# Performance work log

Hardware: AMD Instinct MI355X
Metric: run time of the kernel (lower is better)

The kernel has to match this reference:

```python
import jax, jax.numpy as jnp
import numpy as np

HIDDEN = 1024
HEADS = 16
HEAD_DIM = HIDDEN // HEADS  # 64
BATCH = 2
SEQ = 2048
MASK_IDENTITY = True


def setup_inputs() -> dict:
    key = jax.random.key(0)
    ks = jax.random.split(key, 9)
    s = 1.0 / np.sqrt(HIDDEN)
    return {
        "hidden_states": jax.random.normal(ks[0], (BATCH, SEQ, HIDDEN), jnp.float32),
        "Wq": jax.random.normal(ks[1], (HIDDEN, HIDDEN), jnp.float32) * s,
        "bq": jnp.zeros((HIDDEN,), jnp.float32),
        "Wk": jax.random.normal(ks[2], (HIDDEN, HIDDEN), jnp.float32) * s,
        "bk": jnp.zeros((HIDDEN,), jnp.float32),
        "Wv": jax.random.normal(ks[3], (HIDDEN, HIDDEN), jnp.float32) * s,
        "bv": jnp.zeros((HIDDEN,), jnp.float32),
        "Wd": jax.random.normal(ks[4], (HIDDEN, HIDDEN), jnp.float32) * s,
        "bd": jnp.zeros((HIDDEN,), jnp.float32),
    }


def _split_heads(x):
    # [B, S, H*Dh] -> [B, H, S, Dh]
    b, s, _ = x.shape
    return x.reshape(b, s, HEADS, HEAD_DIM).transpose(0, 2, 1, 3)


def reference(hidden_states, Wq, bq, Wk, bk, Wv, bv, Wd, bd):
    # torch Linear: y = x @ W.T + b
    q = _split_heads(hidden_states @ Wq.T + bq)  # [B,H,S,Dh]
    k = _split_heads(hidden_states @ Wk.T + bk)
    v = _split_heads(hidden_states @ Wv.T + bv)

    scores = jnp.einsum("bhqd,bhkd->bhqk", q, k) / np.sqrt(HEAD_DIM)
    if MASK_IDENTITY:
        mask_value = -jnp.finfo(scores.dtype).max
        eye = jnp.eye(scores.shape[-1], dtype=bool)  # [S,S], broadcast over B,H
        scores = jnp.where(eye, mask_value, scores)
    probs = jax.nn.softmax(scores, axis=-1)
    ctx = jnp.einsum("bhqk,bhkd->bhqd", probs, v)  # [B,H,S,Dh]
    b, h, s, d = ctx.shape
    ctx = ctx.transpose(0, 2, 1, 3).reshape(b, s, h * d)  # [B,S,H*Dh]
    return ctx @ Wd.T + bd
```

## Files before the change

kernel.cpp:

```cpp
#include <hip/hip_runtime.h>
#include <hip/hip_bf16.h>
#include <stdint.h>

#define HIDDEN 1024
#define SEQL   2048
#define NB     2
#define NH     16
#define DH     64
#define MTOT   (NB * SEQL)
#define QKVLD  3072
#define SCALE_Q 0.18033688011112042f

typedef __bf16 bf16x8 __attribute__((ext_vector_type(8)));
typedef __bf16 bf16x4 __attribute__((ext_vector_type(4)));
typedef float  f32x4  __attribute__((ext_vector_type(4)));
typedef float  f32x16 __attribute__((ext_vector_type(16)));

__device__ __forceinline__ void gload16(const void* g, void* l) {
    __builtin_amdgcn_global_load_lds(
        (const __attribute__((address_space(1))) void*)g,
        (__attribute__((address_space(3))) void*)l, 16, 0, 0);
}
__device__ __forceinline__ float exp2fast(float x) {
    float r;
    asm("v_exp_f32 %0, %1" : "=v"(r) : "v"(x));
    return r;
}
__device__ __forceinline__ unsigned cvtpk(float lo, float hi) {
    unsigned r;
    asm("v_cvt_pk_bf16_f32 %0, %1, %2" : "=v"(r) : "v"(lo), "v"(hi));
    return r;
}
__device__ __forceinline__ void pswap(unsigned& a, unsigned& b) {
    asm volatile("v_permlane32_swap_b32 %0, %1" : "+v"(a), "+v"(b));
}

__global__ void prep(const float* __restrict__ H,
                     const float* __restrict__ Wq, const float* __restrict__ Wk,
                     const float* __restrict__ Wv, const float* __restrict__ Wd,
                     const float* __restrict__ bq, const float* __restrict__ bk,
                     const float* __restrict__ bv,
                     __bf16* __restrict__ Hb, __bf16* __restrict__ Wall,
                     float* __restrict__ bqkv) {
    const int bid = blockIdx.x, tid = threadIdx.x;
    if (bid < 4096) {
        int i = bid * 256 + tid;
        float4 v = reinterpret_cast<const float4*>(H)[i];
        bf16x4 o = { (__bf16)v.x, (__bf16)v.y, (__bf16)v.z, (__bf16)v.w };
        reinterpret_cast<bf16x4*>(Hb)[i] = o;
    } else if (bid < 8192) {
        int wi = bid - 4096;
        int seg = wi >> 10;
        int i = (wi & 1023) * 256 + tid;
        const float* src = seg == 0 ? Wq : seg == 1 ? Wk : seg == 2 ? Wv : Wd;
        float sc = (seg == 0) ? SCALE_Q : 1.0f;
        float4 v = reinterpret_cast<const float4*>(src)[i];
        bf16x4 o = { (__bf16)(v.x * sc), (__bf16)(v.y * sc),
                     (__bf16)(v.z * sc), (__bf16)(v.w * sc) };
        reinterpret_cast<bf16x4*>(Wall)[(size_t)seg * 262144 + i] = o;
    } else {
        for (int i = tid; i < 3072; i += 256) {
            float v = (i < 1024) ? bq[i] * SCALE_Q
                    : (i < 2048) ? bk[i - 1024] : bv[i - 2048];
            bqkv[i] = v;
        }
    }
}

__global__ __launch_bounds__(256) void transpose_v(const __bf16* __restrict__ QKV,
                                                   __bf16* __restrict__ Vt) {
    __shared__ __bf16 t[64][66];
    const int st = blockIdx.x, bh = blockIdx.y;
    const int b = bh >> 4, h = bh & 15;
    const int tid = threadIdx.x;
    const int r = tid >> 3, c = tid & 7;
    const __bf16* src = QKV + (size_t)(b * SEQL + st * 64) * QKVLD + 2048 + h * 64;
    *(int4*)&t[r][c * 8]      = *(const int4*)(src + (size_t)r * QKVLD + c * 8);
    *(int4*)&t[r + 32][c * 8] = *(const int4*)(src + (size_t)(r + 32) * QKVLD + c * 8);
    __syncthreads();
    __bf16* dst = Vt + (size_t)bh * DH * SEQL + st * 64;
    const int d = tid >> 3;
    __bf16 tmp0[8], tmp1[8];
#pragma unroll
    for (int j = 0; j < 8; ++j) {
        tmp0[j] = t[c * 8 + j][d];
        tmp1[j] = t[c * 8 + j][d + 32];
    }
    *(int4*)(dst + (size_t)d * SEQL + c * 8)        = *(int4*)tmp0;
    *(int4*)(dst + (size_t)(d + 32) * SEQL + c * 8) = *(int4*)tmp1;
}

__global__ __launch_bounds__(256) void gemm_qkv(const __bf16* __restrict__ A,
                                                const __bf16* __restrict__ Bw,
                                                const float* __restrict__ bias,
                                                __bf16* __restrict__ C) {
    __shared__ __bf16 As[128 * 64];
    __shared__ __bf16 Bs[128 * 64];
    const int K = 1024, N = QKVLD;

    int bid = blockIdx.x;
    int swz = (bid & 7) * 96 + (bid >> 3);
    const int bm = (swz & 31) * 128;
    const int bn = (swz >> 5) * 128;

    const int tid = threadIdx.x;
    const int w = tid >> 6, l = tid & 63, g = l >> 4, lc = l & 15;
    const int wr = (w >> 1) * 64, wc = (w & 1) * 64;

    const int sr = l >> 3;
    const int scol = ((l & 7) ^ sr) * 8;
    const __bf16* Ap = A  + (size_t)(bm + w * 8 + sr) * K + scol;
    const __bf16* Bp = Bw + (size_t)(bn + w * 8 + sr) * K + scol;

    const int rswa = (lc & 7) * 8;

    f32x4 acc[4][4];
    const f32x4 z4 = {0.f, 0.f, 0.f, 0.f};
#pragma unroll
    for (int i = 0; i < 4; ++i)
#pragma unroll
        for (int j = 0; j < 4; ++j) acc[i][j] = z4;

    for (int kt = 0; kt < K; kt += 64) {
#pragma unroll
        for (int q = 0; q < 4; ++q) {
            gload16(Ap + kt + (size_t)(32 * q) * K, &As[(w * 8 + 32 * q) * 64]);
            gload16(Bp + kt + (size_t)(32 * q) * K, &Bs[(w * 8 + 32 * q) * 64]);
        }
        __syncthreads();

        bf16x8 af[4][2], bfr[4][2];
#pragma unroll
        for (int i = 0; i < 4; ++i) {
            const int ra = (wr + i * 16 + lc) * 64;
            const int rb = (wc + i * 16 + lc) * 64;
#pragma unroll
            for (int kk = 0; kk < 2; ++kk) {
                af[i][kk]  = *(const bf16x8*)&As[ra + ((kk * 32 + g * 8) ^ rswa)];
                bfr[i][kk] = *(const bf16x8*)&Bs[rb + ((kk * 32 + g * 8) ^ rswa)];
            }
        }
        __builtin_amdgcn_s_setprio(1);
#pragma unroll
        for (int kk = 0; kk < 2; ++kk)
#pragma unroll
            for (int i = 0; i < 4; ++i)
#pragma unroll
                for (int j = 0; j < 4; ++j)
                    acc[i][j] = __builtin_amdgcn_mfma_f32_16x16x32_bf16(af[i][kk], bfr[j][kk], acc[i][j], 0, 0, 0);
        __builtin_amdgcn_s_setprio(0);
        __syncthreads();
    }

#pragma unroll
    for (int i = 0; i < 4; ++i) {
        int r0 = bm + wr + i * 16 + g * 4;
#pragma unroll
        for (int j = 0; j < 4; ++j) {
            int c = bn + wc + j * 16 + lc;
            float bb = bias[c];
#pragma unroll
            for (int r = 0; r < 4; ++r)
                C[(size_t)(r0 + r) * N + c] = (__bf16)(acc[i][j][r] + bb);
        }
    }
}

__global__ __launch_bounds__(256) void gemm_out(const __bf16* __restrict__ A,
                                                const __bf16* __restrict__ Bw,
                                                const float* __restrict__ bias,
                                                float* __restrict__ Cout) {
    __shared__ __bf16 As[64 * 32];
    __shared__ __bf16 Bs[128 * 32];
    const int K = 1024, N = 1024;

    int bid = blockIdx.x;
    int swz = (bid & 7) * 64 + (bid >> 3);
    const int bm = (swz & 63) * 64;
    const int bn = (swz >> 6) * 128;

    const int tid = threadIdx.x;
    const int w = tid >> 6, l = tid & 63, g = l >> 4, lc = l & 15;
    const int wr = (w >> 1) * 32, wc = (w & 1) * 64;
    const int row = tid >> 2, ch = tid & 3;

    const __bf16* Ap = A  + (size_t)(bm + row) * K + ch * 8;
    const __bf16* Bp = Bw + (size_t)(bn + row) * K + ch * 8;
    __bf16* AsW  = &As[w * 512];
    __bf16* BsLo = &Bs[w * 512];
    __bf16* BsHi = &Bs[2048 + w * 512];

    f32x4 acc[2][4];
    const f32x4 z4 = {0.f, 0.f, 0.f, 0.f};
#pragma unroll
    for (int i = 0; i < 2; ++i)
#pragma unroll
        for (int j = 0; j < 4; ++j) acc[i][j] = z4;

    for (int kt = 0; kt < K; kt += 32) {
        gload16(Ap + kt,                   AsW);
        gload16(Bp + kt,                   BsLo);
        gload16(Bp + kt + (size_t)64 * K,  BsHi);
        __syncthreads();

        bf16x8 af[2], bfr[4];
#pragma unroll
        for (int i = 0; i < 2; ++i)
            af[i] = *(const bf16x8*)&As[(wr + i * 16 + lc) * 32 + g * 8];
#pragma unroll
        for (int j = 0; j < 4; ++j)
            bfr[j] = *(const bf16x8*)&Bs[(wc + j * 16 + lc) * 32 + g * 8];
        __builtin_amdgcn_s_setprio(1);
#pragma unroll
        for (int i = 0; i < 2; ++i)
#pragma unroll
            for (int j = 0; j < 4; ++j)
                acc[i][j] = __builtin_amdgcn_mfma_f32_16x16x32_bf16(af[i], bfr[j], acc[i][j], 0, 0, 0);
        __builtin_amdgcn_s_setprio(0);
        __syncthreads();
    }

#pragma unroll
    for (int i = 0; i < 2; ++i) {
        int r0 = bm + wr + i * 16 + g * 4;
#pragma unroll
        for (int j = 0; j < 4; ++j) {
            int c = bn + wc + j * 16 + lc;
            float bb = bias[c];
#pragma unroll
            for (int r = 0; r < 4; ++r)
                Cout[(size_t)(r0 + r) * N + c] = acc[i][j][r] + bb;
        }
    }
}

__global__ __launch_bounds__(256) void attn_kernel(const __bf16* __restrict__ QKV,
                                                   const __bf16* __restrict__ Vt,
                                                   __bf16* __restrict__ Ctx) {
    __shared__ __bf16 k_lds[2][128][64];
    __shared__ __bf16 v_lds[2][64][128];
    __shared__ float  bc[4][32];

    const int tid = threadIdx.x;
    const int w  = tid >> 6;
    const int l  = tid & 63;
    const int ql = l & 31;
    const int lh = l >> 5;

    int bid = blockIdx.x;
    int swz = (bid & 7) * 64 + (bid >> 3);
    const int qt = swz & 15, bh = swz >> 4;
    const int b = bh >> 4, hd = bh & 15;
    const int qw = qt * 128 + w * 32;

    const __bf16* Qg = QKV + (size_t)b * SEQL * QKVLD + hd * DH;
    const __bf16* Kg = Qg + 1024;
    const __bf16* Vg = Vt + (size_t)bh * DH * SEQL;

    bf16x8 qf[4];
    {
        const __bf16* qp = Qg + (size_t)(qw + ql) * QKVLD + lh * 8;
#pragma unroll
        for (int c = 0; c < 4; ++c) qf[c] = *(const bf16x8*)(qp + c * 16);
    }

    const int sr   = l >> 3;
    const int gcol = ((l & 7) ^ sr) * 8;
    const int vr  = l >> 4;
    const int vch = l & 15;

    auto stage = [&](int kb, int nb) {
#pragma unroll
        for (int q = 0; q < 4; ++q) {
            gload16(Kg + (size_t)(kb + w * 8 + 32 * q + sr) * QKVLD + gcol,
                    &k_lds[nb][w * 8 + 32 * q][0]);
        }
#pragma unroll
        for (int q = 0; q < 4; ++q) {
            int drow = w * 16 + 4 * q + vr;
            int vchunk = vch ^ (drow & 7);
            gload16(Vg + (size_t)drow * SEQL + kb + vchunk * 8,
                    &v_lds[nb][w * 16 + 4 * q][0]);
        }
    };

    stage(0, 0);
    __syncthreads();

    f32x16 o0, o1;
#pragma unroll
    for (int r = 0; r < 16; ++r) { o0[r] = 0.f; o1[r] = 0.f; }
    float l8[8];
#pragma unroll
    for (int r = 0; r < 8; ++r) l8[r] = 0.f;

    f32x16 zc;
#pragma unroll
    for (int r = 0; r < 16; ++r) zc[r] = 0.f;

    const int NT = SEQL / 128;
    const int rsw = (ql & 7) << 3;

    for (int kt = 0; kt < NT; ++kt) {
        const int buf = kt & 1;
        const int kb = kt * 128;

        if (kt + 1 < NT) stage(kb + 128, buf ^ 1);

#pragma unroll
        for (int sub = 0; sub < 2; ++sub) {
            const int kbs = kb + sub * 64;
            const int ro  = sub * 64;

            f32x16 sA, sB;
            __builtin_amdgcn_s_setprio(1);
            {
                bf16x8 k0 = *(const bf16x8*)&k_lds[buf][ro + ql]     [(lh * 8) ^ rsw];
                bf16x8 k1 = *(const bf16x8*)&k_lds[buf][ro + 32 + ql][(lh * 8) ^ rsw];
                sA = __builtin_amdgcn_mfma_f32_32x32x16_bf16(k0, qf[0], zc, 0, 0, 0);
                sB = __builtin_amdgcn_mfma_f32_32x32x16_bf16(k1, qf[0], zc, 0, 0, 0);
            }
#pragma unroll
            for (int c = 1; c < 4; ++c) {
                bf16x8 k0 = *(const bf16x8*)&k_lds[buf][ro + ql]     [(c * 16 + lh * 8) ^ rsw];
                bf16x8 k1 = *(const bf16x8*)&k_lds[buf][ro + 32 + ql][(c * 16 + lh * 8) ^ rsw];
                sA = __builtin_amdgcn_mfma_f32_32x32x16_bf16(k0, qf[c], sA, 0, 0, 0);
                sB = __builtin_amdgcn_mfma_f32_32x32x16_bf16(k1, qf[c], sB, 0, 0, 0);
            }
            __builtin_amdgcn_s_setprio(0);

            if (kbs < qw + 32 && qw < kbs + 64) {
                const int qg = qw + ql;
#pragma unroll
                for (int i = 0; i < 16; ++i) {
                    int kg = kbs + (i & 3) + ((i >> 2) & 3) * 8 + lh * 4;
                    if (kg == qg)      sA[i] = -1e30f;
                    if (kg + 32 == qg) sB[i] = -1e30f;
                }
            }

#pragma unroll
            for (int i = 0; i < 16; ++i) sA[i] = exp2fast(sA[i]);
#pragma unroll
            for (int i = 0; i < 16; ++i) sB[i] = exp2fast(sB[i]);
#pragma unroll
            for (int i = 0; i < 8; ++i)
                l8[i] += (sA[i] + sA[i + 8]) + (sB[i] + sB[i + 8]);

            bf16x8 pa[4];
            {
                unsigned w0 = cvtpk(sA[0],  sA[1]);
                unsigned w1 = cvtpk(sA[2],  sA[3]);
                unsigned w2 = cvtpk(sA[4],  sA[5]);
                unsigned w3 = cvtpk(sA[6],  sA[7]);
                unsigned w4 = cvtpk(sA[8],  sA[9]);
                unsigned w5 = cvtpk(sA[10], sA[11]);
                unsigned w6 = cvtpk(sA[12], sA[13]);
                unsigned w7 = cvtpk(sA[14], sA[15]);
                pswap(w0, w2); pswap(w1, w3);
                pswap(w4, w6); pswap(w5, w7);
                uint4 lo4 = {w0, w1, w2, w3};
                uint4 hi4 = {w4, w5, w6, w7};
                pa[0] = *(bf16x8*)&lo4;
                pa[1] = *(bf16x8*)&hi4;
            }
            {
                unsigned w0 = cvtpk(sB[0],  sB[1]);
                unsigned w1 = cvtpk(sB[2],  sB[3]);
                unsigned w2 = cvtpk(sB[4],  sB[5]);
                unsigned w3 = cvtpk(sB[6],  sB[7]);
                unsigned w4 = cvtpk(sB[8],  sB[9]);
                unsigned w5 = cvtpk(sB[10], sB[11]);
                unsigned w6 = cvtpk(sB[12], sB[13]);
                unsigned w7 = cvtpk(sB[14], sB[15]);
                pswap(w0, w2); pswap(w1, w3);
                pswap(w4, w6); pswap(w5, w7);
                uint4 lo4 = {w0, w1, w2, w3};
                uint4 hi4 = {w4, w5, w6, w7};
                pa[2] = *(bf16x8*)&lo4;
                pa[3] = *(bf16x8*)&hi4;
            }

            __builtin_amdgcn_s_setprio(1);
#pragma unroll
            for (int s = 0; s < 2; ++s)
#pragma unroll
                for (int sl = 0; sl < 2; ++sl) {
                    const int col = sub * 64 + s * 32 + sl * 16 + lh * 8;
                    bf16x8 v0 = *(const bf16x8*)&v_lds[buf][ql]     [col ^ rsw];
                    bf16x8 v1 = *(const bf16x8*)&v_lds[buf][32 + ql][col ^ rsw];
                    o0 = __builtin_amdgcn_mfma_f32_32x32x16_bf16(pa[s * 2 + sl], v0, o0, 0, 0, 0);
                    o1 = __builtin_amdgcn_mfma_f32_32x32x16_bf16(pa[s * 2 + sl], v1, o1, 0, 0, 0);
                }
            __builtin_amdgcn_s_setprio(0);
        }

        __syncthreads();
    }

    float l_r = ((l8[0] + l8[1]) + (l8[2] + l8[3]))
              + ((l8[4] + l8[5]) + (l8[6] + l8[7]));
    l_r += __shfl_xor(l_r, 32, 64);
    if (lh == 0) bc[w][ql] = 1.f / l_r;
    asm volatile("s_waitcnt lgkmcnt(0)" ::: "memory");
    __builtin_amdgcn_wave_barrier();
#pragma unroll
    for (int r = 0; r < 16; ++r) {
        int cr = (r & 3) + (r >> 2) * 8 + lh * 4;
        float iv = bc[w][cr];
        int qrow = qw + cr;
        __bf16* cp = Ctx + (size_t)(b * SEQL + qrow) * HIDDEN + hd * DH + ql;
        cp[0]  = (__bf16)(o0[r] * iv);
        cp[32] = (__bf16)(o1[r] * iv);
    }
}

extern "C" void kernel_launch(void* const* d_in, const int* in_sizes, int n_in,
                              void* d_out, int out_size, void* d_ws, size_t ws_size,
                              hipStream_t stream) {
    const float* H  = (const float*)d_in[0];
    const float* Wq = (const float*)d_in[1];
    const float* bq = (const float*)d_in[2];
    const float* Wk = (const float*)d_in[3];
    const float* bk = (const float*)d_in[4];
    const float* Wv = (const float*)d_in[5];
    const float* bv = (const float*)d_in[6];
    const float* Wd = (const float*)d_in[7];
    const float* bd = (const float*)d_in[8];
    float* out = (float*)d_out;

    char* ws = (char*)d_ws;
    const size_t MB = 1024 * 1024;
    __bf16* Hb    = (__bf16*)(ws + 0 * MB);
    __bf16* Ctx   = (__bf16*)(ws + 0 * MB);
    __bf16* Wqkvb = (__bf16*)(ws + 8 * MB);
    __bf16* Wdb   = (__bf16*)(ws + 14 * MB);
    float*  bqkv  = (float*) (ws + 16 * MB);
    __bf16* QKV   = (__bf16*)(ws + 17 * MB);
    __bf16* Vtb   = (__bf16*)(ws + 41 * MB);
    if (ws_size < 49 * MB) return;

    prep<<<8193, 256, 0, stream>>>(H, Wq, Wk, Wv, Wd, bq, bk, bv, Hb, Wqkvb, bqkv);

    gemm_qkv<<<768, 256, 0, stream>>>(Hb, Wqkvb, bqkv, QKV);

    transpose_v<<<dim3(32, 32), 256, 0, stream>>>(QKV, Vtb);

    attn_kernel<<<512, 256, 0, stream>>>(QKV, Vtb, Ctx);

    gemm_out<<<512, 256, 0, stream>>>(Ctx, Wdb, bd, out);
}
```

Before: 128.6 us.

## Double per-wave query rows in attention; shrink QKV GEMM K-tile to 32

The attention kernel now has each wave handle 64 query rows (two 32-row groups) instead of 32, so every K/V fragment read from shared memory feeds twice as many MFMAs. The grid is halved to 256 blocks of 256 queries each. Separately, the QKV GEMM now stages 32-wide K tiles without the XOR swizzle, halving shared memory but doubling the number of barrier iterations. Risks include higher register pressure in attention, only 256 blocks to fill the device, and possible LDS bank conflicts in the GEMM.

```diff
diff --git a/kernel.cpp b/kernel.cpp
--- a/kernel.cpp
+++ b/kernel.cpp
@@ -94,8 +94,8 @@
                                                 const __bf16* __restrict__ Bw,
                                                 const float* __restrict__ bias,
                                                 __bf16* __restrict__ C) {
-    __shared__ __bf16 As[128 * 64];
-    __shared__ __bf16 Bs[128 * 64];
+    __shared__ __bf16 As[128 * 32];
+    __shared__ __bf16 Bs[128 * 32];
     const int K = 1024, N = QKVLD;
 
     int bid = blockIdx.x;
@@ -106,13 +106,14 @@
     const int tid = threadIdx.x;
     const int w = tid >> 6, l = tid & 63, g = l >> 4, lc = l & 15;
     const int wr = (w >> 1) * 64, wc = (w & 1) * 64;
-
-    const int sr = l >> 3;
-    const int scol = ((l & 7) ^ sr) * 8;
-    const __bf16* Ap = A  + (size_t)(bm + w * 8 + sr) * K + scol;
-    const __bf16* Bp = Bw + (size_t)(bn + w * 8 + sr) * K + scol;
-
-    const int rswa = (lc & 7) * 8;
+    const int row = tid >> 2, ch = tid & 3;
+
+    const __bf16* Ap = A  + (size_t)(bm + row) * K + ch * 8;
+    const __bf16* Bp = Bw + (size_t)(bn + row) * K + ch * 8;
+    __bf16* AsLo = &As[w * 512];
+    __bf16* AsHi = &As[2048 + w * 512];
+    __bf16* BsLo = &Bs[w * 512];
+    __bf16* BsHi = &Bs[2048 + w * 512];
 
     f32x4 acc[4][4];
     const f32x4 z4 = {0.f, 0.f, 0.f, 0.f};
@@ -121,33 +122,26 @@
 #pragma unroll
         for (int j = 0; j < 4; ++j) acc[i][j] = z4;
 
-    for (int kt = 0; kt < K; kt += 64) {
-#pragma unroll
-        for (int q = 0; q < 4; ++q) {
-            gload16(Ap + kt + (size_t)(32 * q) * K, &As[(w * 8 + 32 * q) * 64]);
-            gload16(Bp + kt + (size_t)(32 * q) * K, &Bs[(w * 8 + 32 * q) * 64]);
-        }
+    for (int kt = 0; kt < K; kt += 32) {
+        gload16(Ap + kt,                   AsLo);
+        gload16(Ap + kt + (size_t)64 * K,  AsHi);
+        gload16(Bp + kt,                   BsLo);
+        gload16(Bp + kt + (size_t)64 * K,  BsHi);
         __syncthreads();
 
-        bf16x8 af[4][2], bfr[4][2];
-#pragma unroll
-        for (int i = 0; i < 4; ++i) {
-            const int ra = (wr + i * 16 + lc) * 64;
-            const int rb = (wc + i * 16 + lc) * 64;
-#pragma unroll
-            for (int kk = 0; kk < 2; ++kk) {
-                af[i][kk]  = *(const bf16x8*)&As[ra + ((kk * 32 + g * 8) ^ rswa)];
-                bfr[i][kk] = *(const bf16x8*)&Bs[rb + ((kk * 32 + g * 8) ^ rswa)];
-            }
-        }
+        bf16x8 af[4], bfr[4];
+#pragma unroll
+        for (int i = 0; i < 4; ++i)
+            af[i] = *(const bf16x8*)&As[(wr + i * 16 + lc) * 32 + g * 8];
+#pragma unroll
+        for (int j = 0; j < 4; ++j)
+            bfr[j] = *(const bf16x8*)&Bs[(wc + j * 16 + lc) * 32 + g * 8];
         __builtin_amdgcn_s_setprio(1);
 #pragma unroll
-        for (int kk = 0; kk < 2; ++kk)
-#pragma unroll
-            for (int i = 0; i < 4; ++i)
-#pragma unroll
-                for (int j = 0; j < 4; ++j)
-                    acc[i][j] = __builtin_amdgcn_mfma_f32_16x16x32_bf16(af[i][kk], bfr[j][kk], acc[i][j], 0, 0, 0);
+        for (int i = 0; i < 4; ++i)
+#pragma unroll
+            for (int j = 0; j < 4; ++j)
+                acc[i][j] = __builtin_amdgcn_mfma_f32_16x16x32_bf16(af[i], bfr[j], acc[i][j], 0, 0, 0);
         __builtin_amdgcn_s_setprio(0);
         __syncthreads();
     }
@@ -239,7 +233,7 @@
                                                    __bf16* __restrict__ Ctx) {
     __shared__ __bf16 k_lds[2][128][64];
     __shared__ __bf16 v_lds[2][64][128];
-    __shared__ float  bc[4][32];
+    __shared__ float  bc[4][64];
 
     const int tid = threadIdx.x;
     const int w  = tid >> 6;
@@ -248,27 +242,30 @@
     const int lh = l >> 5;
 
     int bid = blockIdx.x;
-    int swz = (bid & 7) * 64 + (bid >> 3);
-    const int qt = swz & 15, bh = swz >> 4;
+    int swz = (bid & 7) * 32 + (bid >> 3);
+    const int qt = swz & 7, bh = swz >> 3;
     const int b = bh >> 4, hd = bh & 15;
-    const int qw = qt * 128 + w * 32;
+    const int qw = qt * 256 + w * 64;
 
     const __bf16* Qg = QKV + (size_t)b * SEQL * QKVLD + hd * DH;
     const __bf16* Kg = Qg + 1024;
     const __bf16* Vg = Vt + (size_t)bh * DH * SEQL;
 
-    bf16x8 qf[4];
+    bf16x8 qfa[4], qfb[4];
     {
-        const __bf16* qp = Qg + (size_t)(qw + ql) * QKVLD + lh * 8;
-#pragma unroll
-        for (int c = 0; c < 4; ++c) qf[c] = *(const bf16x8*)(qp + c * 16);
+        const __bf16* qp0 = Qg + (size_t)(qw + ql) * QKVLD + lh * 8;
+        const __bf16* qp1 = Qg + (size_t)(qw + 32 + ql) * QKVLD + lh * 8;
+#pragma unroll
+        for (int c = 0; c < 4; ++c) {
+            qfa[c] = *(const bf16x8*)(qp0 + c * 16);
+            qfb[c] = *(const bf16x8*)(qp1 + c * 16);
+        }
     }
 
     const int sr   = l >> 3;
     const int gcol = ((l & 7) ^ sr) * 8;
     const int vr  = l >> 4;
     const int vch = l & 15;
-
     auto stage = [&](int kb, int nb) {
 #pragma unroll
         for (int q = 0; q < 4; ++q) {
@@ -287,12 +284,12 @@
     stage(0, 0);
     __syncthreads();
 
-    f32x16 o0, o1;
-#pragma unroll
-    for (int r = 0; r < 16; ++r) { o0[r] = 0.f; o1[r] = 0.f; }
-    float l8[8];
-#pragma unroll
-    for (int r = 0; r < 8; ++r) l8[r] = 0.f;
+    f32x16 oa0, oa1, ob0, ob1;
+#pragma unroll
+    for (int r = 0; r < 16; ++r) { oa0[r] = 0.f; oa1[r] = 0.f; ob0[r] = 0.f; ob1[r] = 0.f; }
+    float l8a[8], l8b[8];
+#pragma unroll
+    for (int r = 0; r < 8; ++r) { l8a[r] = 0.f; l8b[r] = 0.f; }
 
     f32x16 zc;
 #pragma unroll
@@ -312,20 +309,25 @@
             const int kbs = kb + sub * 64;
             const int ro  = sub * 64;
 
-            f32x16 sA, sB;
+            bf16x8 kf0[4], kf1[4];
+#pragma unroll
+            for (int c = 0; c < 4; ++c) {
+                kf0[c] = *(const bf16x8*)&k_lds[buf][ro + ql]     [(c * 16 + lh * 8) ^ rsw];
+                kf1[c] = *(const bf16x8*)&k_lds[buf][ro + 32 + ql][(c * 16 + lh * 8) ^ rsw];
+            }
+
+            f32x16 sA0, sB0, sA1, sB1;
             __builtin_amdgcn_s_setprio(1);
-            {
-                bf16x8 k0 = *(const bf16x8*)&k_lds[buf][ro + ql]     [(lh * 8) ^ rsw];
-                bf16x8 k1 = *(const bf16x8*)&k_lds[buf][ro + 32 + ql][(lh * 8) ^ rsw];
-                sA = __builtin_amdgcn_mfma_f32_32x32x16_bf16(k0, qf[0], zc, 0, 0, 0);
-                sB = __builtin_amdgcn_mfma_f32_32x32x16_bf16(k1, qf[0], zc, 0, 0, 0);
-            }
+            sA0 = __builtin_amdgcn_mfma_f32_32x32x16_bf16(kf0[0], qfa[0], zc, 0, 0, 0);
+            sB0 = __builtin_amdgcn_mfma_f32_32x32x16_bf16(kf1[0], qfa[0], zc, 0, 0, 0);
+            sA1 = __builtin_amdgcn_mfma_f32_32x32x16_bf16(kf0[0], qfb[0], zc, 0, 0, 0);
+            sB1 = __builtin_amdgcn_mfma_f32_32x32x16_bf16(kf1[0], qfb[0], zc, 0, 0, 0);
 #pragma unroll
             for (int c = 1; c < 4; ++c) {
-                bf16x8 k0 = *(const bf16x8*)&k_lds[buf][ro + ql]     [(c * 16 + lh * 8) ^ rsw];
-                bf16x8 k1 = *(const bf16x8*)&k_lds[buf][ro + 32 + ql][(c * 16 + lh * 8) ^ rsw];
-                sA = __builtin_amdgcn_mfma_f32_32x32x16_bf16(k0, qf[c], sA, 0, 0, 0);
-                sB = __builtin_amdgcn_mfma_f32_32x32x16_bf16(k1, qf[c], sB, 0, 0, 0);
+                sA0 = __builtin_amdgcn_mfma_f32_32x32x16_bf16(kf0[c], qfa[c], sA0, 0, 0, 0);
+                sB0 = __builtin_amdgcn_mfma_f32_32x32x16_bf16(kf1[c], qfa[c], sB0, 0, 0, 0);
+                sA1 = __builtin_amdgcn_mfma_f32_32x32x16_bf16(kf0[c], qfb[c], sA1, 0, 0, 0);
+                sB1 = __builtin_amdgcn_mfma_f32_32x32x16_bf16(kf1[c], qfb[c], sB1, 0, 0, 0);
             }
             __builtin_amdgcn_s_setprio(0);
 
@@ -334,51 +336,102 @@
 #pragma unroll
                 for (int i = 0; i < 16; ++i) {
                     int kg = kbs + (i & 3) + ((i >> 2) & 3) * 8 + lh * 4;
-                    if (kg == qg)      sA[i] = -1e30f;
-                    if (kg + 32 == qg) sB[i] = -1e30f;
+                    if (kg == qg)      sA0[i] = -1e30f;
+                    if (kg + 32 == qg) sB0[i] = -1e30f;
                 }
             }
-
-#pragma unroll
-            for (int i = 0; i < 16; ++i) sA[i] = exp2fast(sA[i]);
-#pragma unroll
-            for (int i = 0; i < 16; ++i) sB[i] = exp2fast(sB[i]);
+            if (kbs < qw + 64 && qw + 32 < kbs + 64) {
+                const int qg = qw + 32 + ql;
+#pragma unroll
+                for (int i = 0; i < 16; ++i) {
+                    int kg = kbs + (i & 3) + ((i >> 2) & 3) * 8 + lh * 4;
+                    if (kg == qg)      sA1[i] = -1e30f;
+                    if (kg + 32 == qg) sB1[i] = -1e30f;
+                }
+            }
+
+#pragma unroll
+            for (int i = 0; i < 16; ++i) sA0[i] = exp2fast(sA0[i]);
+#pragma unroll
+            for (int i = 0; i < 16; ++i) sB0[i] = exp2fast(sB0[i]);
 #pragma unroll
             for (int i = 0; i < 8; ++i)
-                l8[i] += (sA[i] + sA[i + 8]) + (sB[i] + sB[i + 8]);
-
-            bf16x8 pa[4];
+                l8a[i] += (sA0[i] + sA0[i + 8]) + (sB0[i] + sB0[i + 8]);
+
+            bf16x8 pa0[4];
             {
-                unsigned w0 = cvtpk(sA[0],  sA[1]);
-                unsigned w1 = cvtpk(sA[2],  sA[3]);
-                unsigned w2 = cvtpk(sA[4],  sA[5]);
-                unsigned w3 = cvtpk(sA[6],  sA[7]);
-                unsigned w4 = cvtpk(sA[8],  sA[9]);
-                unsigned w5 = cvtpk(sA[10], sA[11]);
-                unsigned w6 = cvtpk(sA[12], sA[13]);
-                unsigned w7 = cvtpk(sA[14], sA[15]);
+                unsigned w0 = cvtpk(sA0[0],  sA0[1]);
+                unsigned w1 = cvtpk(sA0[2],  sA0[3]);
+                unsigned w2 = cvtpk(sA0[4],  sA0[5]);
+                unsigned w3 = cvtpk(sA0[6],  sA0[7]);
+                unsigned w4 = cvtpk(sA0[8],  sA0[9]);
+                unsigned w5 = cvtpk(sA0[10], sA0[11]);
+                unsigned w6 = cvtpk(sA0[12], sA0[13]);
+                unsigned w7 = cvtpk(sA0[14], sA0[15]);
                 pswap(w0, w2); pswap(w1, w3);
                 pswap(w4, w6); pswap(w5, w7);
                 uint4 lo4 = {w0, w1, w2, w3};
                 uint4 hi4 = {w4, w5, w6, w7};
-                pa[0] = *(bf16x8*)&lo4;
-                pa[1] = *(bf16x8*)&hi4;
+                pa0[0] = *(bf16x8*)&lo4;
+                pa0[1] = *(bf16x8*)&hi4;
             }
             {
-                unsigned w0 = cvtpk(sB[0],  sB[1]);
-                unsigned w1 = cvtpk(sB[2],  sB[3]);
-                unsigned w2 = cvtpk(sB[4],  sB[5]);
-                unsigned w3 = cvtpk(sB[6],  sB[7]);
-                unsigned w4 = cvtpk(sB[8],  sB[9]);
-                unsigned w5 = cvtpk(sB[10], sB[11]);
-                unsigned w6 = cvtpk(sB[12], sB[13]);
-                unsigned w7 = cvtpk(sB[14], sB[15]);
+                unsigned w0 = cvtpk(sB0[0],  sB0[1]);
+                unsigned w1 = cvtpk(sB0[2],  sB0[3]);
+                unsigned w2 = cvtpk(sB0[4],  sB0[5]);
+                unsigned w3 = cvtpk(sB0[6],  sB0[7]);
+                unsigned w4 = cvtpk(sB0[8],  sB0[9]);
+                unsigned w5 = cvtpk(sB0[10], sB0[11]);
+                unsigned w6 = cvtpk(sB0[12], sB0[13]);
+                unsigned w7 = cvtpk(sB0[14], sB0[15]);
                 pswap(w0, w2); pswap(w1, w3);
                 pswap(w4, w6); pswap(w5, w7);
                 uint4 lo4 = {w0, w1, w2, w3};
                 uint4 hi4 = {w4, w5, w6, w7};
-                pa[2] = *(bf16x8*)&lo4;
-                pa[3] = *(bf16x8*)&hi4;
+                pa0[2] = *(bf16x8*)&lo4;
+                pa0[3] = *(bf16x8*)&hi4;
+            }
+
+#pragma unroll
+            for (int i = 0; i < 16; ++i) sA1[i] = exp2fast(sA1[i]);
+#pragma unroll
+            for (int i = 0; i < 16; ++i) sB1[i] = exp2fast(sB1[i]);
+#pragma unroll
+            for (int i = 0; i < 8; ++i)
+                l8b[i] += (sA1[i] + sA1[i + 8]) + (sB1[i] + sB1[i + 8]);
+
+            bf16x8 pa1[4];
+            {
+                unsigned w0 = cvtpk(sA1[0],  sA1[1]);
+                unsigned w1 = cvtpk(sA1[2],  sA1[3]);
+                unsigned w2 = cvtpk(sA1[4],  sA1[5]);
+                unsigned w3 = cvtpk(sA1[6],  sA1[7]);
+                unsigned w4 = cvtpk(sA1[8],  sA1[9]);
+                unsigned w5 = cvtpk(sA1[10], sA1[11]);
+                unsigned w6 = cvtpk(sA1[12], sA1[13]);
+                unsigned w7 = cvtpk(sA1[14], sA1[15]);
+                pswap(w0, w2); pswap(w1, w3);
+                pswap(w4, w6); pswap(w5, w7);
+                uint4 lo4 = {w0, w1, w2, w3};
+                uint4 hi4 = {w4, w5, w6, w7};
+                pa1[0] = *(bf16x8*)&lo4;
+                pa1[1] = *(bf16x8*)&hi4;
+            }
+            {
+                unsigned w0 = cvtpk(sB1[0],  sB1[1]);
+                unsigned w1 = cvtpk(sB1[2],  sB1[3]);
+                unsigned w2 = cvtpk(sB1[4],  sB1[5]);
+                unsigned w3 = cvtpk(sB1[6],  sB1[7]);
+                unsigned w4 = cvtpk(sB1[8],  sB1[9]);
+                unsigned w5 = cvtpk(sB1[10], sB1[11]);
+                unsigned w6 = cvtpk(sB1[12], sB1[13]);
+                unsigned w7 = cvtpk(sB1[14], sB1[15]);
+                pswap(w0, w2); pswap(w1, w3);
+                pswap(w4, w6); pswap(w5, w7);
+                uint4 lo4 = {w0, w1, w2, w3};
+                uint4 hi4 = {w4, w5, w6, w7};
+                pa1[2] = *(bf16x8*)&lo4;
+                pa1[3] = *(bf16x8*)&hi4;
             }
 
             __builtin_amdgcn_s_setprio(1);
@@ -389,8 +442,10 @@
                     const int col = sub * 64 + s * 32 + sl * 16 + lh * 8;
                     bf16x8 v0 = *(const bf16x8*)&v_lds[buf][ql]     [col ^ rsw];
                     bf16x8 v1 = *(const bf16x8*)&v_lds[buf][32 + ql][col ^ rsw];
-                    o0 = __builtin_amdgcn_mfma_f32_32x32x16_bf16(pa[s * 2 + sl], v0, o0, 0, 0, 0);
-                    o1 = __builtin_amdgcn_mfma_f32_32x32x16_bf16(pa[s * 2 + sl], v1, o1, 0, 0, 0);
+                    oa0 = __builtin_amdgcn_mfma_f32_32x32x16_bf16(pa0[s * 2 + sl], v0, oa0, 0, 0, 0);
+                    oa1 = __builtin_amdgcn_mfma_f32_32x32x16_bf16(pa0[s * 2 + sl], v1, oa1, 0, 0, 0);
+                    ob0 = __builtin_amdgcn_mfma_f32_32x32x16_bf16(pa1[s * 2 + sl], v0, ob0, 0, 0, 0);
+                    ob1 = __builtin_amdgcn_mfma_f32_32x32x16_bf16(pa1[s * 2 + sl], v1, ob1, 0, 0, 0);
                 }
             __builtin_amdgcn_s_setprio(0);
         }
@@ -398,20 +453,29 @@
         __syncthreads();
     }
 
-    float l_r = ((l8[0] + l8[1]) + (l8[2] + l8[3]))
-              + ((l8[4] + l8[5]) + (l8[6] + l8[7]));
-    l_r += __shfl_xor(l_r, 32, 64);
-    if (lh == 0) bc[w][ql] = 1.f / l_r;
+    float la = ((l8a[0] + l8a[1]) + (l8a[2] + l8a[3]))
+             + ((l8a[4] + l8a[5]) + (l8a[6] + l8a[7]));
+    float lb = ((l8b[0] + l8b[1]) + (l8b[2] + l8b[3]))
+             + ((l8b[4] + l8b[5]) + (l8b[6] + l8b[7]));
+    la += __shfl_xor(la, 32, 64);
+    lb += __shfl_xor(lb, 32, 64);
+    if (lh == 0) {
+        bc[w][ql]      = 1.f / la;
+        bc[w][32 + ql] = 1.f / lb;
+    }
     asm volatile("s_waitcnt lgkmcnt(0)" ::: "memory");
     __builtin_amdgcn_wave_barrier();
 #pragma unroll
     for (int r = 0; r < 16; ++r) {
         int cr = (r & 3) + (r >> 2) * 8 + lh * 4;
-        float iv = bc[w][cr];
-        int qrow = qw + cr;
-        __bf16* cp = Ctx + (size_t)(b * SEQL + qrow) * HIDDEN + hd * DH + ql;
-        cp[0]  = (__bf16)(o0[r] * iv);
-        cp[32] = (__bf16)(o1[r] * iv);
+        float iva = bc[w][cr];
+        float ivb = bc[w][32 + cr];
+        __bf16* cpa = Ctx + (size_t)(b * SEQL + qw + cr) * HIDDEN + hd * DH + ql;
+        __bf16* cpb = Ctx + (size_t)(b * SEQL + qw + 32 + cr) * HIDDEN + hd * DH + ql;
+        cpa[0]  = (__bf16)(oa0[r] * iva);
+        cpa[32] = (__bf16)(oa1[r] * iva);
+        cpb[0]  = (__bf16)(ob0[r] * ivb);
+        cpb[32] = (__bf16)(ob1[r] * ivb);
     }
 }
 
@@ -446,7 +510,7 @@
 
     transpose_v<<<dim3(32, 32), 256, 0, stream>>>(QKV, Vtb);
 
-    attn_kernel<<<512, 256, 0, stream>>>(QKV, Vtb, Ctx);
+    attn_kernel<<<256, 256, 0, stream>>>(QKV, Vtb, Ctx);
 
     gemm_out<<<512, 256, 0, stream>>>(Ctx, Wdb, bd, out);
 }
```

New measurement: 134.6 us. 1.05x slower.
